# Kernel tuning notes

Hardware: AMD Instinct MI355X
Metric: run time of the kernel (lower is better)

The kernel has to match this reference:

```python
import jax, jax.numpy as jnp
import numpy as np

D_MODEL = 2048
N_HEADS = 16
N_KV = 4
HEAD_DIM = D_MODEL // N_HEADS  # 128
KV_DIM = N_KV * HEAD_DIM       # 512
CLIP = 8.0
EPS = 1e-5
THETA = 500000.0


def setup_inputs() -> dict:
    key = jax.random.key(0)
    ks = jax.random.split(key, 12)
    B, T = 2, 2048
    std = 0.02
    return {
        "x": jax.random.normal(ks[0], (B, T, D_MODEL), jnp.float32),
        "wq": jax.random.normal(ks[1], (D_MODEL, D_MODEL), jnp.float32) * std,
        "bq": jnp.zeros((D_MODEL,), jnp.float32),
        "wk": jax.random.normal(ks[2], (KV_DIM, D_MODEL), jnp.float32) * std,
        "bk": jnp.zeros((KV_DIM,), jnp.float32),
        "wv": jax.random.normal(ks[3], (KV_DIM, D_MODEL), jnp.float32) * std,
        "bv": jnp.zeros((KV_DIM,), jnp.float32),
        "wo": jax.random.normal(ks[4], (D_MODEL, D_MODEL), jnp.float32) * std,
        "bo": jnp.zeros((D_MODEL,), jnp.float32),
        "q_gamma": jnp.ones((D_MODEL,), jnp.float32),
        "q_beta": jnp.zeros((D_MODEL,), jnp.float32),
        "k_gamma": jnp.ones((KV_DIM,), jnp.float32),
        "k_beta": jnp.zeros((KV_DIM,), jnp.float32),
    }


def _layernorm(x, gamma, beta):
    mu = jnp.mean(x, axis=-1, keepdims=True)
    var = jnp.mean(jnp.square(x - mu), axis=-1, keepdims=True)
    return (x - mu) * jax.lax.rsqrt(var + EPS) * gamma + beta


def _rope(q, k):
    # q: (B,T,H,Dh), k: (B,T,Hkv,Dh); non-interleaved rotate-half RoPE
    T = q.shape[1]
    half = HEAD_DIM // 2
    inv_freq = 1.0 / (THETA ** (jnp.arange(0, half, dtype=jnp.float32) * 2.0 / HEAD_DIM))
    freqs = jnp.arange(T, dtype=jnp.float32)[:, None] * inv_freq[None, :]  # (T, half)
    emb = jnp.concatenate([freqs, freqs], axis=-1)  # (T, Dh)
    cos = jnp.cos(emb)[None, :, None, :]
    sin = jnp.sin(emb)[None, :, None, :]

    def rot_half(x):
        x1, x2 = x[..., :half], x[..., half:]
        return jnp.concatenate([-x2, x1], axis=-1)

    q = q * cos + rot_half(q) * sin
    k = k * cos + rot_half(k) * sin
    return q, k


def reference(x, wq, bq, wk, bk, wv, bv, wo, bo, q_gamma, q_beta, k_gamma, k_beta):
    B, T, _ = x.shape
    q = x @ wq.T + bq            # (B,T,D)
    k = x @ wk.T + bk            # (B,T,KV_DIM)
    v = x @ wv.T + bv
    q = jnp.clip(q, -CLIP, CLIP)
    k = jnp.clip(k, -CLIP, CLIP)
    v = jnp.clip(v, -CLIP, CLIP)
    q = _layernorm(q, q_gamma, q_beta)
    k = _layernorm(k, k_gamma, k_beta)
    q = q.reshape(B, T, N_HEADS, HEAD_DIM)
    k = k.reshape(B, T, N_KV, HEAD_DIM)
    v = v.reshape(B, T, N_KV, HEAD_DIM)
    q, k = _rope(q, k)
    # to (B,H,T,Dh)
    q = q.transpose(0, 2, 1, 3)
    k = k.transpose(0, 2, 1, 3)
    v = v.transpose(0, 2, 1, 3)
    g = N_HEADS // N_KV
    # GQA repeat_interleave via broadcast: (B,Hkv,T,Dh) -> (B,H,T,Dh)
    k = jnp.broadcast_to(k[:, :, None], (B, N_KV, g, T, HEAD_DIM)).reshape(B, N_HEADS, T, HEAD_DIM)
    v = jnp.broadcast_to(v[:, :, None], (B, N_KV, g, T, HEAD_DIM)).reshape(B, N_HEADS, T, HEAD_DIM)
    scale = 1.0 / jnp.sqrt(jnp.float32(HEAD_DIM))
    scores = jnp.einsum('bhqd,bhkd->bhqk', q, k) * scale
    causal = jnp.tril(jnp.ones((T, T), dtype=bool))
    scores = jnp.where(causal[None, None], scores, jnp.finfo(scores.dtype).min)
    att = jax.nn.softmax(scores, axis=-1)
    out = jnp.einsum('bhqk,bhkd->bhqd', att, v)     # (B,H,T,Dh)
    out = out.transpose(0, 2, 1, 3).reshape(B, T, D_MODEL)
    return out @ wo.T + bo
```

## Files before the change

### kernel.cpp

```cpp
#include <hip/hip_runtime.h>
#include <hip/hip_bf16.h>
#include <math.h>

typedef __bf16 bf16;
typedef __attribute__((ext_vector_type(8))) bf16 bf16x8;
typedef __attribute__((ext_vector_type(2))) bf16 bf16x2;
typedef __attribute__((ext_vector_type(4))) float f32x4;

#define LOG2E 1.4426950408889634f
#define LOG2_THETA 18.931568569324174f

#if __has_builtin(__builtin_amdgcn_exp2f)
#define EXP2F __builtin_amdgcn_exp2f
#else
#define EXP2F exp2f
#endif

__device__ inline void async_cp16(const void* gptr, void* lptr) {
  __builtin_amdgcn_global_load_lds(
      (const __attribute__((address_space(1))) unsigned int*)gptr,
      (__attribute__((address_space(3))) unsigned int*)lptr, 16, 0, 0);
}

__global__ __launch_bounds__(256) void cast_all(
    const float* __restrict__ x,  const float* __restrict__ wq,
    const float* __restrict__ wk, const float* __restrict__ wv,
    const float* __restrict__ wo, bf16* __restrict__ xb,
    bf16* __restrict__ wqkvb, bf16* __restrict__ wob) {
  const int bx = blockIdx.x;
  const size_t gi = ((size_t)bx * 256 + threadIdx.x) * 8;
  const float* src;
  bf16* dst;
  if (bx < 4096)      { src = x  + gi;              dst = xb + gi; }
  else if (bx < 6144) { src = wq + (gi -  8388608); dst = wqkvb + (gi - 8388608); }
  else if (bx < 6656) { src = wk + (gi - 12582912); dst = wqkvb + 4194304 + (gi - 12582912); }
  else if (bx < 7168) { src = wv + (gi - 13631488); dst = wqkvb + 5242880 + (gi - 13631488); }
  else                { src = wo + (gi - 14680064); dst = wob + (gi - 14680064); }
  float4 a = *(const float4*)(src);
  float4 b = *(const float4*)(src + 4);
  bf16x8 o;
  o[0] = (bf16)a.x; o[1] = (bf16)a.y; o[2] = (bf16)a.z; o[3] = (bf16)a.w;
  o[4] = (bf16)b.x; o[5] = (bf16)b.y; o[6] = (bf16)b.z; o[7] = (bf16)b.w;
  *(bf16x8*)dst = o;
}

template <typename OUT_T, bool QKV, bool CLIP>
__global__ __launch_bounds__(256) void gemm_bt(
    const bf16* __restrict__ A, const bf16* __restrict__ W,
    const float* __restrict__ b0, const float* __restrict__ b1,
    const float* __restrict__ b2, OUT_T* __restrict__ C,
    int M, int N, int K) {
  __shared__ bf16 As[128 * 64];
  __shared__ bf16 Bs[128 * 64];
  const int m0 = blockIdx.x * 128, n0 = blockIdx.y * 128;
  const int t = threadIdx.x;
  const int w = t >> 6, lane = t & 63, quad = lane >> 4, l15 = lane & 15;
  const int sw = l15 & 7;
  const int wm = (w >> 1) * 64, wn = (w & 1) * 64;

  f32x4 acc[4][4];
#pragma unroll
  for (int i = 0; i < 4; i++)
#pragma unroll
    for (int j = 0; j < 4; j++) acc[i][j] = (f32x4)0.0f;

  int soff[4];
#pragma unroll
  for (int i = 0; i < 4; i++) {
    const int c = w * 256 + i * 64 + lane;
    const int r = c >> 3;
    const int sl = (c & 7) ^ (r & 7);
    soff[i] = r * K + sl * 8;
  }
  const bf16* Abase = A + (size_t)m0 * K;
  const bf16* Wbase = W + (size_t)n0 * K;

  for (int k0 = 0; k0 < K; k0 += 64) {
#pragma unroll
    for (int i = 0; i < 4; i++) {
      const int dst = (w * 256 + i * 64) * 16;
      async_cp16(Abase + k0 + soff[i], (char*)As + dst);
      async_cp16(Wbase + k0 + soff[i], (char*)Bs + dst);
    }
    __syncthreads();

#pragma unroll
    for (int kk = 0; kk < 2; kk++) {
      bf16x8 af[4], bfr[4];
#pragma unroll
      for (int i = 0; i < 4; i++)
        af[i] = *(const bf16x8*)(As + (wm + i * 16 + l15) * 64 +
                                 (((kk * 4 + quad) ^ sw) * 8));
#pragma unroll
      for (int j = 0; j < 4; j++)
        bfr[j] = *(const bf16x8*)(Bs + (wn + j * 16 + l15) * 64 +
                                  (((kk * 4 + quad) ^ sw) * 8));
#pragma unroll
      for (int i = 0; i < 4; i++)
#pragma unroll
        for (int j = 0; j < 4; j++)
          acc[i][j] = __builtin_amdgcn_mfma_f32_16x16x32_bf16(af[i], bfr[j], acc[i][j], 0, 0, 0);
    }
    __syncthreads();
  }

#pragma unroll
  for (int i = 0; i < 4; i++)
#pragma unroll
    for (int j = 0; j < 4; j++) {
      const int col = n0 + wn + j * 16 + l15;
      float bval;
      if (QKV) {
        if (col < 2048) bval = b0[col];
        else if (col < 2560) bval = b1[col - 2048];
        else bval = b2[col - 2560];
      } else {
        bval = b0[col];
      }
#pragma unroll
      for (int r = 0; r < 4; r++) {
        const int row = m0 + wm + i * 16 + quad * 4 + r;
        float v = acc[i][j][r] + bval;
        if (CLIP) v = fminf(fmaxf(v, -8.0f), 8.0f);
        C[(size_t)row * N + col] = (OUT_T)v;
      }
    }
}

__global__ __launch_bounds__(256) void fused_mid(
    const bf16* __restrict__ X, const float* __restrict__ qg,
    const float* __restrict__ qb, const float* __restrict__ kg,
    const float* __restrict__ kb, bf16* __restrict__ Qr,
    bf16* __restrict__ Kr, bf16* __restrict__ Vt) {
  __shared__ float smf[2056];
  __shared__ bf16 smt[64][136];
  const int bx = blockIdx.x;
  const int tid = threadIdx.x;
  const int w = tid >> 6, lane = tid & 63;
  float* red = smf + 2048;

  if (bx < 4096) {
    const int row = bx, b = row >> 11, tpos = row & 2047;
    const bf16* x = X + (size_t)row * 3072;
    bf16x8 xi = *(const bf16x8*)(x + tid * 8);
    float v[8];
    float s = 0.0f;
#pragma unroll
    for (int e = 0; e < 8; e++) { v[e] = (float)xi[e]; s += v[e]; }
#pragma unroll
    for (int m = 32; m >= 1; m >>= 1) s += __shfl_xor(s, m, 64);
    if (lane == 0) red[w] = s;
    __syncthreads();
    const float mean = (red[0] + red[1] + red[2] + red[3]) * (1.0f / 2048.0f);
    float vs = 0.0f;
#pragma unroll
    for (int e = 0; e < 8; e++) { float d = v[e] - mean; vs += d * d; }
#pragma unroll
    for (int m = 32; m >= 1; m >>= 1) vs += __shfl_xor(vs, m, 64);
    if (lane == 0) red[4 + w] = vs;
    __syncthreads();
    const float var = (red[4] + red[5] + red[6] + red[7]) * (1.0f / 2048.0f);
    const float rstd = rsqrtf(var + 1e-5f);
#pragma unroll
    for (int e = 0; e < 8; e++) {
      const int c = tid * 8 + e;
      const float y = (v[e] - mean) * rstd * qg[c] + qb[c];
      smf[c] = y; v[e] = y;
    }
    __syncthreads();
    const int c0 = tid * 8;
    const int h = c0 >> 7;
    bf16x8 ov;
#pragma unroll
    for (int e = 0; e < 8; e++) {
      const int c = c0 + e, d = c & 127, i = d & 63;
      const float inv = exp2f((float)i * (-LOG2_THETA / 64.0f));
      float sn, cs;
      sincosf((float)tpos * inv, &sn, &cs);
      const float rot = (d < 64) ? -smf[c + 64] : smf[c - 64];
      ov[e] = (bf16)(v[e] * cs + rot * sn);
    }
    *(bf16x8*)(Qr + ((size_t)(b * 16 + h) * 2048 + tpos) * 128 + (c0 & 127)) = ov;
  } else if (bx < 8192) {
    const int row = bx - 4096, b = row >> 11, tpos = row & 2047;
    const bf16* x = X + (size_t)row * 3072 + 2048;
    bf16x2 xi = *(const bf16x2*)(x + tid * 2);
    float v0 = (float)xi[0], v1 = (float)xi[1];
    float s = v0 + v1;
#pragma unroll
    for (int m = 32; m >= 1; m >>= 1) s += __shfl_xor(s, m, 64);
    if (lane == 0) red[w] = s;
    __syncthreads();
    const float mean = (red[0] + red[1] + red[2] + red[3]) * (1.0f / 512.0f);
    float d0 = v0 - mean, d1 = v1 - mean;
    float vs = d0 * d0 + d1 * d1;
#pragma unroll
    for (int m = 32; m >= 1; m >>= 1) vs += __shfl_xor(vs, m, 64);
    if (lane == 0) red[4 + w] = vs;
    __syncthreads();
    const float var = (red[4] + red[5] + red[6] + red[7]) * (1.0f / 512.0f);
    const float rstd = rsqrtf(var + 1e-5f);
    const int c0 = tid * 2;
    float y0 = d0 * rstd * kg[c0] + kb[c0];
    float y1 = d1 * rstd * kg[c0 + 1] + kb[c0 + 1];
    smf[c0] = y0; smf[c0 + 1] = y1;
    __syncthreads();
    const int kv = c0 >> 7;
    float yy[2] = {y0, y1};
    bf16x2 ov;
#pragma unroll
    for (int e = 0; e < 2; e++) {
      const int c = c0 + e, d = c & 127, i = d & 63;
      const float inv = exp2f((float)i * (-LOG2_THETA / 64.0f));
      float sn, cs;
      sincosf((float)tpos * inv, &sn, &cs);
      const float rot = (d < 64) ? -smf[c + 64] : smf[c - 64];
      ov[e] = (bf16)(yy[e] * cs + rot * sn);
    }
    *(bf16x2*)(Kr + ((size_t)(b * 4 + kv) * 2048 + tpos) * 128 + (c0 & 127)) = ov;
  } else {
    const int idx = bx - 8192;
    const int b = idx >> 7, kv = (idx >> 5) & 3, t0 = (idx & 31) * 64;
#pragma unroll
    for (int i = 0; i < 4; i++) {
      const int c = i * 256 + tid;
      const int r = c >> 4, d8 = (c & 15) * 8;
      *(bf16x8*)&smt[r][d8] =
          *(const bf16x8*)(X + (size_t)(b * 2048 + t0 + r) * 3072 + 2560 + kv * 128 + d8);
    }
    __syncthreads();
#pragma unroll
    for (int i = 0; i < 4; i++) {
      const int c = i * 256 + tid;
      const int d = c >> 3, t8 = (c & 7) * 8;
      bf16x8 o;
#pragma unroll
      for (int j = 0; j < 8; j++) o[j] = smt[t8 + j][d];
      *(bf16x8*)(Vt + (size_t)((b * 4 + kv) * 128 + d) * 2048 + t0 + t8) = o;
    }
  }
}

__global__ __launch_bounds__(256) void flash_attn(
    const bf16* __restrict__ Q, const bf16* __restrict__ Kt,
    const bf16* __restrict__ Vt, bf16* __restrict__ O) {
  const int p = blockIdx.x;
  const int h = blockIdx.y, b = blockIdx.z;
  const int kv = h >> 2;
  const int tid = threadIdx.x;
  const int w = tid >> 6, lane = tid & 63, quad = lane >> 4, l15 = lane & 15;

  __shared__ bf16 Ks[64][128];
  __shared__ bf16 Vs[128][64];
  __shared__ bf16 Ps[4][16][88];

  const bf16* Kb = Kt + (size_t)(b * 4 + kv) * 2048 * 128;
  const bf16* Vb = Vt + (size_t)(b * 4 + kv) * 128 * 2048;

  const int ksl = lane & 15, krt = lane >> 4;
  const int vsl = lane & 7,  vdt = lane >> 3;
  int okff[4], ovff[4];
#pragma unroll
  for (int i = 0; i < 4; i++) {
    const int c = w * 4 + i;
    const int rt = c * 4 + krt;
    okff[i] = rt * 128 + ((ksl ^ (rt & 15)) * 8);
    const int d = c * 8 + vdt;
    ovff[i] = d * 2048 + ((vsl ^ (d & 7)) * 8);
  }

  const float cexp = 0.08838834764831845f * LOG2E;
  bf16x8 ones;
#pragma unroll
  for (int i = 0; i < 8; i++) ones[i] = (bf16)1.0f;

#pragma unroll 1
  for (int pass = 0; pass < 2; pass++) {
    const int qb = (pass == 0) ? (31 - p) : p;
    const int q0 = qb * 64;
    const int nkt = qb + 1;

    const bf16* Qb = Q + ((size_t)(b * 16 + h) * 2048 + q0 + w * 16 + l15) * 128;
    bf16x8 aq[4];
#pragma unroll
    for (int kk = 0; kk < 4; kk++) aq[kk] = *(const bf16x8*)(Qb + kk * 32 + quad * 8);

    f32x4 o[9];
#pragma unroll
    for (int dt = 0; dt < 9; dt++) o[dt] = (f32x4)0.0f;

#pragma unroll 1
    for (int kt = 0; kt < nkt; kt++) {
      const int k0 = kt * 64;
      __syncthreads();
      {
        const size_t kbase = (size_t)k0 * 128;
#pragma unroll
        for (int i = 0; i < 4; i++) {
          const int c = w * 4 + i;
          async_cp16(Kb + kbase + okff[i], (char*)&Ks[0][0] + c * 1024);
          async_cp16(Vb + (size_t)k0 + ovff[i], (char*)&Vs[0][0] + c * 1024);
        }
      }
      __syncthreads();

      f32x4 s4[4];
#pragma unroll
      for (int j = 0; j < 4; j++) {
        f32x4 acc = (f32x4)0.0f;
        const int n = j * 16 + l15;
#pragma unroll
        for (int kk = 0; kk < 4; kk++) {
          bf16x8 bk = *(const bf16x8*)(
              &Ks[0][0] + n * 128 + (((kk * 4 + quad) ^ l15) * 8));
          acc = __builtin_amdgcn_mfma_f32_16x16x32_bf16(aq[kk], bk, acc, 0, 0, 0);
        }
        s4[j] = acc;
      }

      const bool diag = (kt == qb);
      const int qrow_base = q0 + w * 16 + quad * 4;
#pragma unroll
      for (int j = 0; j < 4; j++) {
        const int kg = k0 + j * 16 + l15;
#pragma unroll
        for (int r = 0; r < 4; r++) {
          float pv = EXP2F(s4[j][r] * cexp);
          if (diag && kg > qrow_base + r) pv = 0.0f;
          Ps[w][quad * 4 + r][j * 16 + l15] = (bf16)pv;
        }
      }
      __asm__ volatile("s_waitcnt lgkmcnt(0)" ::: "memory");

#pragma unroll
      for (int kk = 0; kk < 2; kk++) {
        bf16x8 pa = *(const bf16x8*)&Ps[w][l15][kk * 32 + quad * 8];
#pragma unroll
        for (int dt = 0; dt < 8; dt++) {
          const int d = dt * 16 + l15;
          bf16x8 vb = *(const bf16x8*)(
              &Vs[0][0] + d * 64 + (((kk * 4 + quad) ^ (d & 7)) * 8));
          o[dt] = __builtin_amdgcn_mfma_f32_16x16x32_bf16(pa, vb, o[dt], 0, 0, 0);
        }
        o[8] = __builtin_amdgcn_mfma_f32_16x16x32_bf16(pa, ones, o[8], 0, 0, 0);
      }
    }

    bf16* Ob = O + ((size_t)(b * 2048 + q0 + w * 16 + quad * 4)) * 2048 + h * 128;
#pragma unroll
    for (int r = 0; r < 4; r++) {
      const float rinv = 1.0f / o[8][r];
#pragma unroll
      for (int dt = 0; dt < 8; dt++)
        Ob[(size_t)r * 2048 + dt * 16 + l15] = (bf16)(o[dt][r] * rinv);
    }
  }
}

extern "C" void kernel_launch(void* const* d_in, const int* in_sizes, int n_in,
                              void* d_out, int out_size, void* d_ws, size_t ws_size,
                              hipStream_t stream) {
  const float* x   = (const float*)d_in[0];
  const float* wq  = (const float*)d_in[1];
  const float* bq  = (const float*)d_in[2];
  const float* wk  = (const float*)d_in[3];
  const float* bk  = (const float*)d_in[4];
  const float* wv  = (const float*)d_in[5];
  const float* bv  = (const float*)d_in[6];
  const float* wo  = (const float*)d_in[7];
  const float* bo  = (const float*)d_in[8];
  const float* qg  = (const float*)d_in[9];
  const float* qbt = (const float*)d_in[10];
  const float* kg  = (const float*)d_in[11];
  const float* kbt = (const float*)d_in[12];
  float* out = (float*)d_out;

  char* ws = (char*)d_ws;
  if (ws_size < (size_t)88080384) return;
  bf16* xb    = (bf16*)(ws);
  bf16* wqkvb = (bf16*)(ws + 16777216);
  bf16* wob   = (bf16*)(ws + 29360128);
  bf16* qkvb  = (bf16*)(ws + 37748736);
  bf16* Qr    = (bf16*)(ws + 62914560);
  bf16* Kr    = (bf16*)(ws + 79691776);
  bf16* Vt    = (bf16*)(ws + 83886080);
  bf16* At    = (bf16*)(ws);

  cast_all<<<9216, 256, 0, stream>>>(x, wq, wk, wv, wo, xb, wqkvb, wob);
  gemm_bt<bf16, true, true><<<dim3(32, 24), 256, 0, stream>>>(
      xb, wqkvb, bq, bk, bv, qkvb, 4096, 3072, 2048);
  fused_mid<<<8448, 256, 0, stream>>>(qkvb, qg, qbt, kg, kbt, Qr, Kr, Vt);
  flash_attn<<<dim3(16, 16, 2), 256, 0, stream>>>(Qr, Kr, Vt, At);
  gemm_bt<float, false, false><<<dim3(32, 16), 256, 0, stream>>>(
      At, wob, bo, nullptr, nullptr, out, 4096, 2048, 2048);
}
```

Baseline: 329.8 us.

## Share KV tiles across two heads, double-buffer loads, keep P in registers

The flash attention kernel now runs 512 threads per block covering two query heads that share one KV head. The K/V tile loaded into LDS is reused by both heads, and a double buffer prefetches the next tile while the current one is computed. The score MFMA is transposed so probabilities can be rearranged with lane shuffles instead of a round trip through LDS, and the output store is vectorised. The shuffles and selects add VALU work, and the larger blocks change occupancy.

```diff
diff --git a/kernel.cpp b/kernel.cpp
--- a/kernel.cpp
+++ b/kernel.cpp
@@ -4,6 +4,7 @@
 
 typedef __bf16 bf16;
 typedef __attribute__((ext_vector_type(8))) bf16 bf16x8;
+typedef __attribute__((ext_vector_type(4))) bf16 bf16x4;
 typedef __attribute__((ext_vector_type(2))) bf16 bf16x2;
 typedef __attribute__((ext_vector_type(4))) float f32x4;
 
@@ -241,118 +242,152 @@
   }
 }
 
-__global__ __launch_bounds__(256) void flash_attn(
+__global__ __launch_bounds__(512) void flash_attn(
     const bf16* __restrict__ Q, const bf16* __restrict__ Kt,
     const bf16* __restrict__ Vt, bf16* __restrict__ O) {
+  __shared__ bf16 Ks[2][64][128];
+  __shared__ bf16 Vs[2][128][64];
+
   const int p = blockIdx.x;
-  const int h = blockIdx.y, b = blockIdx.z;
-  const int kv = h >> 2;
+  const int hp = blockIdx.y;
+  const int b = blockIdx.z;
+  const int kv = hp >> 1;
   const int tid = threadIdx.x;
   const int w = tid >> 6, lane = tid & 63, quad = lane >> 4, l15 = lane & 15;
-
-  __shared__ bf16 Ks[64][128];
-  __shared__ bf16 Vs[128][64];
-  __shared__ bf16 Ps[4][16][88];
+  const int strip = w & 3, hl = w >> 2;
+  const int h = hp * 2 + hl;
 
   const bf16* Kb = Kt + (size_t)(b * 4 + kv) * 2048 * 128;
   const bf16* Vb = Vt + (size_t)(b * 4 + kv) * 128 * 2048;
 
-  const int ksl = lane & 15, krt = lane >> 4;
-  const int vsl = lane & 7,  vdt = lane >> 3;
-  int okff[4], ovff[4];
-#pragma unroll
-  for (int i = 0; i < 4; i++) {
-    const int c = w * 4 + i;
-    const int rt = c * 4 + krt;
-    okff[i] = rt * 128 + ((ksl ^ (rt & 15)) * 8);
-    const int d = c * 8 + vdt;
-    ovff[i] = d * 2048 + ((vsl ^ (d & 7)) * 8);
+  int koff[2], voff[2];
+#pragma unroll
+  for (int i = 0; i < 2; i++) {
+    const int c = w * 128 + i * 64 + lane;
+    const int kr = c >> 4, kp = c & 15;
+    koff[i] = kr * 128 + ((kp ^ (kr & 15)) * 8);
+    const int vd = c >> 3, vp = c & 7;
+    voff[i] = vd * 2048 + ((vp ^ (vd & 7)) * 8);
   }
 
   const float cexp = 0.08838834764831845f * LOG2E;
-  bf16x8 ones;
-#pragma unroll
-  for (int i = 0; i < 8; i++) ones[i] = (bf16)1.0f;
+  bf16x8 onesA;
+#pragma unroll
+  for (int i = 0; i < 8; i++) onesA[i] = (bf16)1.0f;
+
+  const int srcA = l15 + ((quad & 1) << 5);
+  const int srcB = srcA + 16;
+  const bool hiSel = (quad >> 1) != 0;
 
 #pragma unroll 1
   for (int pass = 0; pass < 2; pass++) {
     const int qb = (pass == 0) ? (31 - p) : p;
     const int q0 = qb * 64;
     const int nkt = qb + 1;
-
-    const bf16* Qb = Q + ((size_t)(b * 16 + h) * 2048 + q0 + w * 16 + l15) * 128;
+    const int qrow = q0 + strip * 16 + l15;
+
+    const bf16* Qb = Q + ((size_t)(b * 16 + h) * 2048 + qrow) * 128;
     bf16x8 aq[4];
 #pragma unroll
     for (int kk = 0; kk < 4; kk++) aq[kk] = *(const bf16x8*)(Qb + kk * 32 + quad * 8);
 
-    f32x4 o[9];
-#pragma unroll
-    for (int dt = 0; dt < 9; dt++) o[dt] = (f32x4)0.0f;
+    f32x4 o[8];
+#pragma unroll
+    for (int dt = 0; dt < 8; dt++) o[dt] = (f32x4)0.0f;
+    f32x4 o8 = (f32x4)0.0f;
+
+    __syncthreads();
+#pragma unroll
+    for (int i = 0; i < 2; i++) {
+      const int dst = (w * 128 + i * 64) * 16;
+      async_cp16(Kb + koff[i], (char*)Ks + dst);
+      async_cp16(Vb + voff[i], (char*)Vs + dst);
+    }
 
 #pragma unroll 1
     for (int kt = 0; kt < nkt; kt++) {
       const int k0 = kt * 64;
+      const int cur = kt & 1;
       __syncthreads();
-      {
-        const size_t kbase = (size_t)k0 * 128;
-#pragma unroll
-        for (int i = 0; i < 4; i++) {
-          const int c = w * 4 + i;
-          async_cp16(Kb + kbase + okff[i], (char*)&Ks[0][0] + c * 1024);
-          async_cp16(Vb + (size_t)k0 + ovff[i], (char*)&Vs[0][0] + c * 1024);
+
+      if (kt + 1 < nkt) {
+        const size_t kn = (size_t)(k0 + 64);
+#pragma unroll
+        for (int i = 0; i < 2; i++) {
+          const int dst = (w * 128 + i * 64) * 16;
+          async_cp16(Kb + kn * 128 + koff[i], (char*)Ks + (cur ^ 1) * 16384 + dst);
+          async_cp16(Vb + kn + voff[i], (char*)Vs + (cur ^ 1) * 16384 + dst);
         }
       }
-      __syncthreads();
-
-      f32x4 s4[4];
+
+      const bf16* Kcur = &Ks[cur][0][0];
+      const bf16* Vcur = &Vs[cur][0][0];
+
+      f32x4 s4t[4];
 #pragma unroll
       for (int j = 0; j < 4; j++) {
         f32x4 acc = (f32x4)0.0f;
-        const int n = j * 16 + l15;
+        const int krow = j * 16 + l15;
 #pragma unroll
         for (int kk = 0; kk < 4; kk++) {
-          bf16x8 bk = *(const bf16x8*)(
-              &Ks[0][0] + n * 128 + (((kk * 4 + quad) ^ l15) * 8));
-          acc = __builtin_amdgcn_mfma_f32_16x16x32_bf16(aq[kk], bk, acc, 0, 0, 0);
+          bf16x8 bk = *(const bf16x8*)(Kcur + krow * 128 + (((kk * 4 + quad) ^ l15) * 8));
+          acc = __builtin_amdgcn_mfma_f32_16x16x32_bf16(bk, aq[kk], acc, 0, 0, 0);
         }
-        s4[j] = acc;
+        s4t[j] = acc;
       }
 
       const bool diag = (kt == qb);
-      const int qrow_base = q0 + w * 16 + quad * 4;
+      unsigned pp[4][2];
 #pragma unroll
       for (int j = 0; j < 4; j++) {
-        const int kg = k0 + j * 16 + l15;
+        const int kbase = k0 + j * 16 + quad * 4;
+        float pv[4];
 #pragma unroll
         for (int r = 0; r < 4; r++) {
-          float pv = EXP2F(s4[j][r] * cexp);
-          if (diag && kg > qrow_base + r) pv = 0.0f;
-          Ps[w][quad * 4 + r][j * 16 + l15] = (bf16)pv;
+          float e = EXP2F(s4t[j][r] * cexp);
+          if (diag && (kbase + r > qrow)) e = 0.0f;
+          pv[r] = e;
         }
-      }
-      __asm__ volatile("s_waitcnt lgkmcnt(0)" ::: "memory");
+        union { bf16x2 h; unsigned u; } u0, u1;
+        u0.h[0] = (bf16)pv[0]; u0.h[1] = (bf16)pv[1];
+        u1.h[0] = (bf16)pv[2]; u1.h[1] = (bf16)pv[3];
+        pp[j][0] = u0.u; pp[j][1] = u1.u;
+      }
 
 #pragma unroll
       for (int kk = 0; kk < 2; kk++) {
-        bf16x8 pa = *(const bf16x8*)&Ps[w][l15][kk * 32 + quad * 8];
+        const int ja = 2 * kk, jb = 2 * kk + 1;
+        unsigned a00 = (unsigned)__shfl((int)pp[ja][0], srcA, 64);
+        unsigned a01 = (unsigned)__shfl((int)pp[ja][1], srcA, 64);
+        unsigned a10 = (unsigned)__shfl((int)pp[jb][0], srcA, 64);
+        unsigned a11 = (unsigned)__shfl((int)pp[jb][1], srcA, 64);
+        unsigned b00 = (unsigned)__shfl((int)pp[ja][0], srcB, 64);
+        unsigned b01 = (unsigned)__shfl((int)pp[ja][1], srcB, 64);
+        unsigned b10 = (unsigned)__shfl((int)pp[jb][0], srcB, 64);
+        unsigned b11 = (unsigned)__shfl((int)pp[jb][1], srcB, 64);
+        union { unsigned u[4]; bf16x8 v; } ub;
+        ub.u[0] = hiSel ? a10 : a00;
+        ub.u[1] = hiSel ? a11 : a01;
+        ub.u[2] = hiSel ? b10 : b00;
+        ub.u[3] = hiSel ? b11 : b01;
 #pragma unroll
         for (int dt = 0; dt < 8; dt++) {
           const int d = dt * 16 + l15;
-          bf16x8 vb = *(const bf16x8*)(
-              &Vs[0][0] + d * 64 + (((kk * 4 + quad) ^ (d & 7)) * 8));
-          o[dt] = __builtin_amdgcn_mfma_f32_16x16x32_bf16(pa, vb, o[dt], 0, 0, 0);
+          bf16x8 av = *(const bf16x8*)(Vcur + d * 64 + (((kk * 4 + quad) ^ (d & 7)) * 8));
+          o[dt] = __builtin_amdgcn_mfma_f32_16x16x32_bf16(av, ub.v, o[dt], 0, 0, 0);
         }
-        o[8] = __builtin_amdgcn_mfma_f32_16x16x32_bf16(pa, ones, o[8], 0, 0, 0);
-      }
-    }
-
-    bf16* Ob = O + ((size_t)(b * 2048 + q0 + w * 16 + quad * 4)) * 2048 + h * 128;
-#pragma unroll
-    for (int r = 0; r < 4; r++) {
-      const float rinv = 1.0f / o[8][r];
-#pragma unroll
-      for (int dt = 0; dt < 8; dt++)
-        Ob[(size_t)r * 2048 + dt * 16 + l15] = (bf16)(o[dt][r] * rinv);
+        o8 = __builtin_amdgcn_mfma_f32_16x16x32_bf16(onesA, ub.v, o8, 0, 0, 0);
+      }
+    }
+
+    const float rinv = 1.0f / o8[0];
+    bf16* Ob = O + ((size_t)(b * 2048) + qrow) * 2048 + h * 128;
+#pragma unroll
+    for (int dt = 0; dt < 8; dt++) {
+      bf16x4 pk;
+#pragma unroll
+      for (int r = 0; r < 4; r++) pk[r] = (bf16)(o[dt][r] * rinv);
+      *(bf16x4*)(Ob + dt * 16 + quad * 4) = pk;
     }
   }
 }
@@ -390,7 +425,7 @@
   gemm_bt<bf16, true, true><<<dim3(32, 24), 256, 0, stream>>>(
       xb, wqkvb, bq, bk, bv, qkvb, 4096, 3072, 2048);
   fused_mid<<<8448, 256, 0, stream>>>(qkvb, qg, qbt, kg, kbt, Qr, Kr, Vt);
-  flash_attn<<<dim3(16, 16, 2), 256, 0, stream>>>(Qr, Kr, Vt, At);
+  flash_attn<<<dim3(16, 8, 2), 512, 0, stream>>>(Qr, Kr, Vt, At);
   gemm_bt<float, false, false><<<dim3(32, 16), 256, 0, stream>>>(
       At, wob, bo, nullptr, nullptr, out, 4096, 2048, 2048);
 }
```

Result: no change. 330.9 us (+0.3%).

## Double-buffer K/V tiles in flash attention and launch one query block per workgroup

Applied to the files above, without the earlier changes.

The attention kernel now uses 32-key tiles held in two LDS buffers, so the async global-to-LDS copy for the next tile is issued while the current tile is being computed. Each workgroup now handles a single 64-row query block instead of a balanced pair of blocks, which doubles the grid size. The intent is to hide K/V load latency and raise occupancy through smaller LDS use and more workgroups. The cost is twice as many loop iterations and barriers per query block. Dropping the pairing also removes the causal load balancing, so work per workgroup becomes uneven.

```diff
diff --git a/kernel.cpp b/kernel.cpp
--- a/kernel.cpp
+++ b/kernel.cpp
@@ -4,6 +4,7 @@
 
 typedef __bf16 bf16;
 typedef __attribute__((ext_vector_type(8))) bf16 bf16x8;
+typedef __attribute__((ext_vector_type(4))) bf16 bf16x4;
 typedef __attribute__((ext_vector_type(2))) bf16 bf16x2;
 typedef __attribute__((ext_vector_type(4))) float f32x4;
 
@@ -244,29 +245,27 @@
 __global__ __launch_bounds__(256) void flash_attn(
     const bf16* __restrict__ Q, const bf16* __restrict__ Kt,
     const bf16* __restrict__ Vt, bf16* __restrict__ O) {
-  const int p = blockIdx.x;
+  __shared__ bf16 Ks[2][32][128];
+  __shared__ bf16 Vs[2][128][32];
+  __shared__ bf16 Ps[4][16][44];
+
+  const int qb = 31 - (int)blockIdx.x;
   const int h = blockIdx.y, b = blockIdx.z;
   const int kv = h >> 2;
   const int tid = threadIdx.x;
   const int w = tid >> 6, lane = tid & 63, quad = lane >> 4, l15 = lane & 15;
 
-  __shared__ bf16 Ks[64][128];
-  __shared__ bf16 Vs[128][64];
-  __shared__ bf16 Ps[4][16][88];
-
   const bf16* Kb = Kt + (size_t)(b * 4 + kv) * 2048 * 128;
   const bf16* Vb = Vt + (size_t)(b * 4 + kv) * 128 * 2048;
 
-  const int ksl = lane & 15, krt = lane >> 4;
-  const int vsl = lane & 7,  vdt = lane >> 3;
-  int okff[4], ovff[4];
-#pragma unroll
-  for (int i = 0; i < 4; i++) {
-    const int c = w * 4 + i;
-    const int rt = c * 4 + krt;
-    okff[i] = rt * 128 + ((ksl ^ (rt & 15)) * 8);
-    const int d = c * 8 + vdt;
-    ovff[i] = d * 2048 + ((vsl ^ (d & 7)) * 8);
+  int koff[2], voff[2];
+#pragma unroll
+  for (int i = 0; i < 2; i++) {
+    const int c = tid + 256 * i;
+    const int kr = c >> 4, kp = c & 15;
+    koff[i] = kr * 128 + ((kp ^ (kr & 15)) * 8);
+    const int vd = c >> 2, vp = c & 3;
+    voff[i] = vd * 2048 + ((vp ^ (vd & 3)) * 8);
   }
 
   const float cexp = 0.08838834764831845f * LOG2E;
@@ -274,86 +273,92 @@
 #pragma unroll
   for (int i = 0; i < 8; i++) ones[i] = (bf16)1.0f;
 
+  const int q0 = qb * 64;
+  const int nkt = 2 * (qb + 1);
+  const int qrow_base = q0 + w * 16 + quad * 4;
+
+  const bf16* Qb = Q + ((size_t)(b * 16 + h) * 2048 + q0 + w * 16 + l15) * 128;
+  bf16x8 aq[4];
+#pragma unroll
+  for (int kk = 0; kk < 4; kk++) aq[kk] = *(const bf16x8*)(Qb + kk * 32 + quad * 8);
+
+  f32x4 o[8];
+#pragma unroll
+  for (int dt = 0; dt < 8; dt++) o[dt] = (f32x4)0.0f;
+  f32x4 o8 = (f32x4)0.0f;
+
+#pragma unroll
+  for (int i = 0; i < 2; i++) {
+    const int dst = (tid & 192) * 16 + i * 4096 + 0;
+    async_cp16(Kb + koff[i], (char*)Ks + ((w * 64 + 256 * i) * 16));
+    async_cp16(Vb + voff[i], (char*)Vs + ((w * 64 + 256 * i) * 16));
+    (void)dst;
+  }
+
 #pragma unroll 1
-  for (int pass = 0; pass < 2; pass++) {
-    const int qb = (pass == 0) ? (31 - p) : p;
-    const int q0 = qb * 64;
-    const int nkt = qb + 1;
-
-    const bf16* Qb = Q + ((size_t)(b * 16 + h) * 2048 + q0 + w * 16 + l15) * 128;
-    bf16x8 aq[4];
-#pragma unroll
-    for (int kk = 0; kk < 4; kk++) aq[kk] = *(const bf16x8*)(Qb + kk * 32 + quad * 8);
-
-    f32x4 o[9];
-#pragma unroll
-    for (int dt = 0; dt < 9; dt++) o[dt] = (f32x4)0.0f;
-
-#pragma unroll 1
-    for (int kt = 0; kt < nkt; kt++) {
-      const int k0 = kt * 64;
-      __syncthreads();
-      {
-        const size_t kbase = (size_t)k0 * 128;
-#pragma unroll
-        for (int i = 0; i < 4; i++) {
-          const int c = w * 4 + i;
-          async_cp16(Kb + kbase + okff[i], (char*)&Ks[0][0] + c * 1024);
-          async_cp16(Vb + (size_t)k0 + ovff[i], (char*)&Vs[0][0] + c * 1024);
-        }
-      }
-      __syncthreads();
-
-      f32x4 s4[4];
-#pragma unroll
-      for (int j = 0; j < 4; j++) {
-        f32x4 acc = (f32x4)0.0f;
-        const int n = j * 16 + l15;
-#pragma unroll
-        for (int kk = 0; kk < 4; kk++) {
-          bf16x8 bk = *(const bf16x8*)(
-              &Ks[0][0] + n * 128 + (((kk * 4 + quad) ^ l15) * 8));
-          acc = __builtin_amdgcn_mfma_f32_16x16x32_bf16(aq[kk], bk, acc, 0, 0, 0);
-        }
-        s4[j] = acc;
-      }
-
-      const bool diag = (kt == qb);
-      const int qrow_base = q0 + w * 16 + quad * 4;
-#pragma unroll
-      for (int j = 0; j < 4; j++) {
-        const int kg = k0 + j * 16 + l15;
-#pragma unroll
-        for (int r = 0; r < 4; r++) {
-          float pv = EXP2F(s4[j][r] * cexp);
-          if (diag && kg > qrow_base + r) pv = 0.0f;
-          Ps[w][quad * 4 + r][j * 16 + l15] = (bf16)pv;
-        }
-      }
-      __asm__ volatile("s_waitcnt lgkmcnt(0)" ::: "memory");
-
-#pragma unroll
-      for (int kk = 0; kk < 2; kk++) {
-        bf16x8 pa = *(const bf16x8*)&Ps[w][l15][kk * 32 + quad * 8];
-#pragma unroll
-        for (int dt = 0; dt < 8; dt++) {
-          const int d = dt * 16 + l15;
-          bf16x8 vb = *(const bf16x8*)(
-              &Vs[0][0] + d * 64 + (((kk * 4 + quad) ^ (d & 7)) * 8));
-          o[dt] = __builtin_amdgcn_mfma_f32_16x16x32_bf16(pa, vb, o[dt], 0, 0, 0);
-        }
-        o[8] = __builtin_amdgcn_mfma_f32_16x16x32_bf16(pa, ones, o[8], 0, 0, 0);
-      }
-    }
-
-    bf16* Ob = O + ((size_t)(b * 2048 + q0 + w * 16 + quad * 4)) * 2048 + h * 128;
-#pragma unroll
-    for (int r = 0; r < 4; r++) {
-      const float rinv = 1.0f / o[8][r];
-#pragma unroll
-      for (int dt = 0; dt < 8; dt++)
-        Ob[(size_t)r * 2048 + dt * 16 + l15] = (bf16)(o[dt][r] * rinv);
-    }
+  for (int kt = 0; kt < nkt; kt++) {
+    const int k0 = kt * 32;
+    const int cur = kt & 1;
+    __syncthreads();
+
+    if (kt + 1 < nkt) {
+      const size_t kn = (size_t)(k0 + 32);
+#pragma unroll
+      for (int i = 0; i < 2; i++) {
+        const int dst = (w * 64 + 256 * i) * 16;
+        async_cp16(Kb + kn * 128 + koff[i], (char*)Ks + (cur ^ 1) * 8192 + dst);
+        async_cp16(Vb + kn + voff[i], (char*)Vs + (cur ^ 1) * 8192 + dst);
+      }
+    }
+
+    const bf16* Kcur = &Ks[cur][0][0];
+    const bf16* Vcur = &Vs[cur][0][0];
+
+    f32x4 s4[2];
+#pragma unroll
+    for (int j = 0; j < 2; j++) {
+      f32x4 acc = (f32x4)0.0f;
+      const int krow = j * 16 + l15;
+#pragma unroll
+      for (int kk = 0; kk < 4; kk++) {
+        bf16x8 bk = *(const bf16x8*)(Kcur + krow * 128 + (((kk * 4 + quad) ^ l15) * 8));
+        acc = __builtin_amdgcn_mfma_f32_16x16x32_bf16(aq[kk], bk, acc, 0, 0, 0);
+      }
+      s4[j] = acc;
+    }
+
+    const bool diag = (kt >= nkt - 2);
+#pragma unroll
+    for (int j = 0; j < 2; j++) {
+      const int kg = k0 + j * 16 + l15;
+#pragma unroll
+      for (int r = 0; r < 4; r++) {
+        float pv = EXP2F(s4[j][r] * cexp);
+        if (diag && kg > qrow_base + r) pv = 0.0f;
+        Ps[w][quad * 4 + r][j * 16 + l15] = (bf16)pv;
+      }
+    }
+    __asm__ volatile("s_waitcnt lgkmcnt(0)" ::: "memory");
+
+    {
+      bf16x8 pa = *(const bf16x8*)&Ps[w][l15][quad * 8];
+#pragma unroll
+      for (int dt = 0; dt < 8; dt++) {
+        const int d = dt * 16 + l15;
+        bf16x8 vb = *(const bf16x8*)(Vcur + d * 32 + ((quad ^ (d & 3)) * 8));
+        o[dt] = __builtin_amdgcn_mfma_f32_16x16x32_bf16(pa, vb, o[dt], 0, 0, 0);
+      }
+      o8 = __builtin_amdgcn_mfma_f32_16x16x32_bf16(pa, ones, o8, 0, 0, 0);
+    }
+  }
+
+  bf16* Ob = O + ((size_t)(b * 2048) + q0 + w * 16 + quad * 4) * 2048 + h * 128;
+#pragma unroll
+  for (int r = 0; r < 4; r++) {
+    const float rinv = 1.0f / o8[r];
+#pragma unroll
+    for (int dt = 0; dt < 8; dt++)
+      Ob[(size_t)r * 2048 + dt * 16 + l15] = (bf16)(o[dt][r] * rinv);
   }
 }
 
@@ -390,7 +395,7 @@
   gemm_bt<bf16, true, true><<<dim3(32, 24), 256, 0, stream>>>(
       xb, wqkvb, bq, bk, bv, qkvb, 4096, 3072, 2048);
   fused_mid<<<8448, 256, 0, stream>>>(qkvb, qg, qbt, kg, kbt, Qr, Kr, Vt);
-  flash_attn<<<dim3(16, 16, 2), 256, 0, stream>>>(Qr, Kr, Vt, At);
+  flash_attn<<<dim3(32, 16, 2), 256, 0, stream>>>(Qr, Kr, Vt, At);
   gemm_bt<float, false, false><<<dim3(32, 16), 256, 0, stream>>>(
       At, wob, bo, nullptr, nullptr, out, 4096, 2048, 2048);
 }
```

Measured after the change: 349.1 us. +5.9%, slower.
